# Kernel tuning notes

Measured on AMD Instinct MI355X. Metric: run time of the kernel, lower is better.

Reference implementation:

```python
import jax, jax.numpy as jnp
import numpy as np

B, S, D_IN, D_H, D_OUT, NB = 4, 4096, 1024, 1024, 1024, 8
BD = D_H // NB  # block size of the block-diagonal gate projections
R_MIN, R_MAX, EPS = 0.9, 0.999, 1e-8


def setup_inputs() -> dict:
    key = jax.random.key(0)
    ks = jax.random.split(key, 8)
    x = jax.random.normal(ks[0], (B, S, D_IN), dtype=jnp.float32)
    h0 = jnp.zeros((B, D_H), dtype=jnp.float32)
    # input projection Dense(d_hidden)
    W_in = jax.random.normal(ks[1], (D_IN, D_H), dtype=jnp.float32) / np.sqrt(D_IN)
    b_in = jnp.zeros((D_H,), dtype=jnp.float32)
    # two BlockDiagonalLinear gate projections (n_blocks blocks of [BD, BD])
    Wgx = jax.random.normal(ks[2], (NB, BD, BD), dtype=jnp.float32) / np.sqrt(BD)
    bgx = jnp.zeros((D_H,), dtype=jnp.float32)
    Wga = jax.random.normal(ks[3], (NB, BD, BD), dtype=jnp.float32) / np.sqrt(BD)
    bga = jnp.zeros((D_H,), dtype=jnp.float32)
    # stable_init_real: softplus(param) == -log(r) with r ~ U[r_min, r_max] in magnitude
    u = jax.random.uniform(ks[4], (D_H,), dtype=jnp.float32)
    a_real = 0.5 * jnp.log(u * (R_MAX**2 - R_MIN**2) + R_MIN**2 + EPS)
    a_real_param = jnp.log(jnp.exp(-a_real) - 1.0)
    # output projection Dense(d_out)
    W_out = jax.random.normal(ks[5], (D_H, D_OUT), dtype=jnp.float32) / np.sqrt(D_H)
    b_out = jnp.zeros((D_OUT,), dtype=jnp.float32)
    return dict(x=x, h0=h0, W_in=W_in, b_in=b_in, Wgx=Wgx, bgx=bgx,
                Wga=Wga, bga=bga, a_real_param=a_real_param,
                W_out=W_out, b_out=b_out)


def _block_diag_linear(x, W, b):
    # x: [B,S,D_H] -> split into NB blocks of BD, per-block matmul
    xb = x.reshape(x.shape[0], x.shape[1], NB, BD)
    y = jnp.einsum('bsni,nio->bsno', xb, W)
    return y.reshape(x.shape[0], x.shape[1], D_H) + b


def reference(x, h0, W_in, b_in, Wgx, bgx, Wga, bga, a_real_param, W_out, b_out):
    # input projection
    x = x @ W_in + b_in  # [B,S,D_H]
    # input-dependent gates (sigmoid of block-diagonal projections)
    gate_x = jax.nn.sigmoid(_block_diag_linear(x, Wgx, bgx))
    gate_a = jax.nn.sigmoid(_block_diag_linear(x, Wga, bga))
    # real-only RG-LRU recurrence coefficient: a = exp(-8 * gate_a * softplus(c))
    log_a = -8.0 * gate_a * jax.nn.softplus(a_real_param)  # [B,S,D_H], <= 0
    a = jnp.exp(log_a)
    # gated input with sqrt(1 - a^2) normalization (sqrt_bound_derivative fwd == sqrt)
    gx = gate_x * x * jnp.sqrt(1.0 - jnp.exp(2.0 * log_a))
    # fold initial state into the first step: h_1 = a_1 * h0 + gx_1
    gx = gx.at[:, 0].add(a[:, 0] * h0)
    # linear scan h_t = a_t * h_{t-1} + gx_t via associative scan over seq axis
    def combine(c1, c2):
        a1, x1 = c1
        a2, x2 = c2
        return (a2 * a1, a2 * x1 + x2)
    _, h = jax.lax.associative_scan(combine, (a, gx), axis=1)  # [B,S,D_H]
    out = h @ W_out + b_out  # [B,S,D_OUT]
    return out, h[:, -1]
```

## Files before the change

### kernel.cpp

```cpp
#include <hip/hip_runtime.h>

#define B_SZ 4
#define SEQ 4096
#define DIN 1024
#define DH 1024
#define DOUT 1024
#define NBLK 8
#define MTOK (B_SZ * SEQ)
#define CHUNK 64
#define NCHUNK (SEQ / CHUNK)

typedef _Float16 half8 __attribute__((ext_vector_type(8)));
typedef _Float16 half4v __attribute__((ext_vector_type(4)));
typedef float f32x4 __attribute__((ext_vector_type(4)));

union HPack { unsigned int u; _Float16 h[2]; };

__device__ __forceinline__ void gl_lds16(const void* g, void* l) {
  __builtin_amdgcn_global_load_lds((__attribute__((address_space(1))) void*)g,
                                   (__attribute__((address_space(3))) void*)l,
                                   16, 0, 0);
}

__device__ __forceinline__ int swz_h(int r, int c) {
  return (((r << 8) | (c << 1)) ^ ((r & 7) << 4)) >> 1;
}

__global__ __launch_bounds__(256)
void prep_kernel(const float* __restrict__ Win, const float* __restrict__ Wout,
                 const float* __restrict__ Wgx, const float* __restrict__ Wga,
                 _Float16* __restrict__ WinT, _Float16* __restrict__ WoutT,
                 _Float16* __restrict__ WgxT, _Float16* __restrict__ WgaT) {
  __shared__ float tile[64][65];
  int t = blockIdx.x;
  const float* src; _Float16* dst; int C; size_t bo = 0;
  if (t < 256)      { src = Win;  dst = WinT;  C = 1024; }
  else if (t < 512) { src = Wout; dst = WoutT; C = 1024; t -= 256; }
  else if (t < 544) { int u = t - 512; src = Wgx; dst = WgxT; C = 128;
                      bo = (size_t)(u >> 2) * (128 * 128); t = u & 3; }
  else              { int u = t - 544; src = Wga; dst = WgaT; C = 128;
                      bo = (size_t)(u >> 2) * (128 * 128); t = u & 3; }
  const int nbx = C >> 6;
  const int r0 = (t / nbx) * 64, c0 = (t % nbx) * 64;
  const int tr = threadIdx.x >> 6, tc = threadIdx.x & 63;
#pragma unroll
  for (int i = 0; i < 64; i += 4)
    tile[tr + i][tc] = src[bo + (size_t)(r0 + tr + i) * C + c0 + tc];
  __syncthreads();
#pragma unroll
  for (int i = 0; i < 64; i += 4) {
    const int cc = i + tr;
    dst[bo + (size_t)(c0 + cc) * C + r0 + tc] = (_Float16)tile[tc][cc];
  }
}

template <int OUT_F32>
__global__ __launch_bounds__(256, 4)
void gemm_bt(const _Float16* __restrict__ A, const _Float16* __restrict__ Bt,
             const float* __restrict__ bias, void* __restrict__ C,
             int M, int N, int K) {
  __shared__ __align__(16) _Float16 As[128 * 64];
  __shared__ __align__(16) _Float16 Bs[128 * 64];
  const int tid = threadIdx.x;
  const int wave = tid >> 6, lane = tid & 63;
  const int m0 = blockIdx.x * 128, n0 = blockIdx.y * 128;
  const int wm = (wave >> 1) * 64, wn = (wave & 1) * 64;
  const int row = lane & 15, quad = lane >> 4;
  const int srow = lane >> 3, scol = (lane & 7) * 8;

  f32x4 acc[4][4] = {};
#pragma unroll 1
  for (int kt = 0; kt < K; kt += 64) {
#pragma unroll
    for (int ci = 0; ci < 4; ci++) {
      const int c = wave * 4 + ci;
      gl_lds16(A  + (size_t)(m0 + c * 8 + srow) * K + kt + scol, As + c * 512);
      gl_lds16(Bt + (size_t)(n0 + c * 8 + srow) * K + kt + scol, Bs + c * 512);
    }
    __syncthreads();
#pragma unroll
    for (int kk = 0; kk < 64; kk += 32) {
      half8 af[4], bf[4];
#pragma unroll
      for (int i = 0; i < 4; i++)
        af[i] = *(const half8*)&As[(wm + i * 16 + row) * 64 + kk + quad * 8];
#pragma unroll
      for (int i = 0; i < 4; i++)
        bf[i] = *(const half8*)&Bs[(wn + i * 16 + row) * 64 + kk + quad * 8];
#pragma unroll
      for (int i = 0; i < 4; i++)
#pragma unroll
        for (int j = 0; j < 4; j++)
          acc[i][j] = __builtin_amdgcn_mfma_f32_16x16x32_f16(af[i], bf[j], acc[i][j], 0, 0, 0);
    }
    __syncthreads();
  }
  float bv[4];
#pragma unroll
  for (int j = 0; j < 4; j++) bv[j] = bias[n0 + wn + j * 16 + row];
#pragma unroll
  for (int i = 0; i < 4; i++) {
#pragma unroll
    for (int r = 0; r < 4; r++) {
      const int m = m0 + wm + i * 16 + quad * 4 + r;
      const size_t base = (size_t)m * N + n0 + wn + row;
#pragma unroll
      for (int j = 0; j < 4; j++) {
        const float v = acc[i][j][r] + bv[j];
        if (OUT_F32) ((float*)C)[base + j * 16] = v;
        else         ((_Float16*)C)[base + j * 16] = (_Float16)v;
      }
    }
  }
}

__global__ __launch_bounds__(256, 4)
void gemm1_gates(const float* __restrict__ Ax, const _Float16* __restrict__ Bt,
                 const float* __restrict__ bias,
                 const _Float16* __restrict__ WxT, const _Float16* __restrict__ WaT,
                 const float* __restrict__ bgx, const float* __restrict__ bga,
                 const float* __restrict__ arp,
                 unsigned int* __restrict__ ag,
                 float* __restrict__ cA, float* __restrict__ cH) {
  __shared__ __align__(16) _Float16 smem[128 * 128];
  _Float16* const As = smem;
  _Float16* const Bs = smem + 128 * 64;
  const int tid = threadIdx.x;
  const int wave = tid >> 6, lane = tid & 63;
  const int m0 = blockIdx.x * 128, nb = blockIdx.y, n0 = nb * 128;
  const int wm = (wave >> 1) * 64, wn = (wave & 1) * 64;
  const int row = lane & 15, quad = lane >> 4;
  const int srow = lane >> 3, scol = (lane & 7) * 8;

  f32x4 acc[4][4] = {};
#pragma unroll 1
  for (int kt = 0; kt < DIN; kt += 64) {
#pragma unroll
    for (int ci = 0; ci < 4; ci++) {
      const int c = wave * 4 + ci;
      gl_lds16(Bt + (size_t)(n0 + c * 8 + srow) * DIN + kt + scol, Bs + c * 512);
    }
#pragma unroll
    for (int ci = 0; ci < 4; ci++) {
      const int c = wave * 4 + ci;
      const float* s = Ax + (size_t)(m0 + c * 8 + srow) * DIN + kt + scol;
      const float4 t0 = ((const float4*)s)[0];
      const float4 t1 = ((const float4*)s)[1];
      half8 hv;
      hv[0] = (_Float16)t0.x; hv[1] = (_Float16)t0.y;
      hv[2] = (_Float16)t0.z; hv[3] = (_Float16)t0.w;
      hv[4] = (_Float16)t1.x; hv[5] = (_Float16)t1.y;
      hv[6] = (_Float16)t1.z; hv[7] = (_Float16)t1.w;
      *(half8*)&As[c * 512 + lane * 8] = hv;
    }
    __syncthreads();
#pragma unroll
    for (int kk = 0; kk < 64; kk += 32) {
      half8 af[4], bf[4];
#pragma unroll
      for (int i = 0; i < 4; i++)
        af[i] = *(const half8*)&As[(wm + i * 16 + row) * 64 + kk + quad * 8];
#pragma unroll
      for (int i = 0; i < 4; i++)
        bf[i] = *(const half8*)&Bs[(wn + i * 16 + row) * 64 + kk + quad * 8];
#pragma unroll
      for (int i = 0; i < 4; i++)
#pragma unroll
        for (int j = 0; j < 4; j++)
          acc[i][j] = __builtin_amdgcn_mfma_f32_16x16x32_f16(af[i], bf[j], acc[i][j], 0, 0, 0);
    }
    __syncthreads();
  }

  {
    float bv[4];
#pragma unroll
    for (int j = 0; j < 4; j++) bv[j] = bias[n0 + wn + j * 16 + row];
#pragma unroll
    for (int i = 0; i < 4; i++)
#pragma unroll
      for (int r = 0; r < 4; r++) {
        const int tl = wm + i * 16 + quad * 4 + r;
#pragma unroll
        for (int j = 0; j < 4; j++)
          smem[swz_h(tl, wn + j * 16 + row)] = (_Float16)(acc[i][j][r] + bv[j]);
      }
  }
  __syncthreads();

  const _Float16* const WxB = WxT + (size_t)nb * (128 * 128);
  const _Float16* const WaB = WaT + (size_t)nb * (128 * 128);
  const int b_idx = (m0 + wm) >> 12;
  const int c_idx = ((m0 + wm) & (SEQ - 1)) >> 6;
  const int cbase = c_idx * (B_SZ * DH) + b_idx * DH + n0 + wn + row;
  const size_t agbase = ((size_t)(blockIdx.x * NBLK + nb) * 4 + wave) * 4096;

#pragma unroll 1
  for (int jp = 0; jp < 2; jp++) {
    f32x4 accx[4][2] = {}, acca[4][2] = {};
#pragma unroll
    for (int kk = 0; kk < 128; kk += 32) {
      half8 af[4];
#pragma unroll
      for (int i = 0; i < 4; i++)
        af[i] = *(const half8*)&smem[swz_h(wm + i * 16 + row, kk + quad * 8)];
#pragma unroll
      for (int jj = 0; jj < 2; jj++) {
        const size_t wo = (size_t)(wn + (jp * 2 + jj) * 16 + row) * 128 + kk + quad * 8;
        const half8 bx = *(const half8*)&WxB[wo];
        const half8 ba = *(const half8*)&WaB[wo];
#pragma unroll
        for (int i = 0; i < 4; i++) {
          accx[i][jj] = __builtin_amdgcn_mfma_f32_16x16x32_f16(af[i], bx, accx[i][jj], 0, 0, 0);
          acca[i][jj] = __builtin_amdgcn_mfma_f32_16x16x32_f16(af[i], ba, acca[i][jj], 0, 0, 0);
        }
      }
    }
    float bxv[2], bav[2], cd[2];
#pragma unroll
    for (int jj = 0; jj < 2; jj++) {
      const int d = n0 + wn + (jp * 2 + jj) * 16 + row;
      bxv[jj] = bgx[d]; bav[jj] = bga[d];
      cd[jj] = log1pf(expf(arp[d]));
    }
    float Arun[2] = {1.f, 1.f}, Hrun[2] = {0.f, 0.f};
#pragma unroll
    for (int i = 0; i < 4; i++) {
      float Aseg[2] = {1.f, 1.f}, Hseg[2] = {0.f, 0.f};
#pragma unroll
      for (int r = 0; r < 4; r++) {
        const int tl = wm + i * 16 + quad * 4 + r;
#pragma unroll
        for (int jj = 0; jj < 2; jj++) {
          const float px = accx[i][jj][r] + bxv[jj];
          const float pa = acca[i][jj][r] + bav[jj];
          const float sx = 1.f / (1.f + __expf(-px));
          const float sa = 1.f / (1.f + __expf(-pa));
          const float a = __expf(-8.f * sa * cd[jj]);
          const float n2 = fmaxf(1.f - a * a, 0.f);
          const float xv = (float)smem[swz_h(tl, wn + (jp * 2 + jj) * 16 + row)];
          HPack pk;
          pk.h[0] = (_Float16)a;
          pk.h[1] = (_Float16)(sx * xv * sqrtf(n2));
          ag[agbase + (size_t)(((i * 4 + r) * 4) + jp * 2 + jj) * 64 + lane] = pk.u;
          const float ar = (float)pk.h[0], gr = (float)pk.h[1];
          Aseg[jj] *= ar;
          Hseg[jj] = fmaf(ar, Hseg[jj], gr);
        }
      }
#pragma unroll
      for (int jj = 0; jj < 2; jj++) {
        float A1 = Aseg[jj], H1 = Hseg[jj];
        float A2 = __shfl_down(A1, 16, 64), H2 = __shfl_down(H1, 16, 64);
        H1 = fmaf(A2, H1, H2); A1 *= A2;
        A2 = __shfl_down(A1, 32, 64); H2 = __shfl_down(H1, 32, 64);
        H1 = fmaf(A2, H1, H2); A1 *= A2;
        Hrun[jj] = fmaf(A1, Hrun[jj], H1);
        Arun[jj] *= A1;
      }
    }
    if (lane < 16) {
#pragma unroll
      for (int jj = 0; jj < 2; jj++) {
        cA[cbase + (jp * 2 + jj) * 16] = Arun[jj];
        cH[cbase + (jp * 2 + jj) * 16] = Hrun[jj];
      }
    }
  }
}

__global__ __launch_bounds__(256)
void scan_p2(const float* __restrict__ cA, const float* __restrict__ cH,
             const float* __restrict__ h0, float* __restrict__ cin,
             float* __restrict__ hlast) {
  const int wave = threadIdx.x >> 6, lane = threadIdx.x & 63;
  const int g = blockIdx.x * 4 + wave;
  float A = cA[(size_t)lane * (B_SZ * DH) + g], H = cH[(size_t)lane * (B_SZ * DH) + g];
#pragma unroll
  for (int d = 1; d < 64; d <<= 1) {
    const float Ap = __shfl_up(A, d, 64), Hp = __shfl_up(H, d, 64);
    if (lane >= d) { H = fmaf(A, Hp, H); A *= Ap; }
  }
  const float h0g = h0[g];
  if (lane == 63) hlast[g] = fmaf(A, h0g, H);
  float Ae = __shfl_up(A, 1, 64), He = __shfl_up(H, 1, 64);
  if (lane == 0) { Ae = 1.f; He = 0.f; }
  cin[(size_t)lane * (B_SZ * DH) + g] = fmaf(Ae, h0g, He);
}

__global__ __launch_bounds__(256)
void scan_p3(const unsigned int* __restrict__ ag,
             const float* __restrict__ cin, _Float16* __restrict__ h) {
  const int gtid = blockIdx.x * 256 + threadIdx.x;
  const int d = gtid & (DH - 1);
  const int bc = gtid >> 10;
  const int b = bc >> 6, c = bc & (NCHUNK - 1);
  const int mblk = b * 32 + (c >> 1), wmb = c & 1;
  const int nb = d >> 7, wnb = (d >> 6) & 1, j = (d >> 4) & 3, row = d & 15;
  const size_t agb = ((size_t)(mblk * NBLK + nb) * 4 + wmb * 2 + wnb) * 4096
                   + j * 64 + row;
  const size_t hbase = ((size_t)(b * SEQ + c * CHUNK)) * DH + d;
  float carry = cin[c * (B_SZ * DH) + b * DH + d];
#pragma unroll 8
  for (int t = 0; t < CHUNK; t++) {
    HPack pk;
    pk.u = ag[agb + (size_t)(((t >> 4) * 4 + (t & 3)) * 4) * 64 + ((t >> 2) & 3) * 16];
    const float av = (float)pk.h[0];
    const float gv = (float)pk.h[1];
    carry = fmaf(av, carry, gv);
    h[hbase + (size_t)t * DH] = (_Float16)carry;
  }
}

extern "C" void kernel_launch(void* const* d_in, const int* in_sizes, int n_in,
                              void* d_out, int out_size, void* d_ws, size_t ws_size,
                              hipStream_t stream) {
  const float* x     = (const float*)d_in[0];
  const float* h0    = (const float*)d_in[1];
  const float* W_in  = (const float*)d_in[2];
  const float* b_in  = (const float*)d_in[3];
  const float* Wgx   = (const float*)d_in[4];
  const float* bgx   = (const float*)d_in[5];
  const float* Wga   = (const float*)d_in[6];
  const float* bga   = (const float*)d_in[7];
  const float* arp   = (const float*)d_in[8];
  const float* W_out = (const float*)d_in[9];
  const float* b_out = (const float*)d_in[10];
  float* out = (float*)d_out;
  float* hlast = out + (size_t)MTOK * DOUT;

  char* p = (char*)d_ws;
  auto take = [&](size_t bytes) { char* r = p; p += (bytes + 255) & ~(size_t)255; return r; };
  _Float16* h_buf = (_Float16*)take((size_t)MTOK * DH * 2);
  unsigned int* ag = (unsigned int*)take((size_t)MTOK * DH * 4);
  _Float16* WinT  = (_Float16*)take((size_t)DIN * DH * 2);
  _Float16* WoutT = (_Float16*)take((size_t)DH * DOUT * 2);
  _Float16* WgxT  = (_Float16*)take((size_t)NBLK * 128 * 128 * 2);
  _Float16* WgaT  = (_Float16*)take((size_t)NBLK * 128 * 128 * 2);
  float* cA   = (float*)take((size_t)NCHUNK * B_SZ * DH * 4);
  float* cH   = (float*)take((size_t)NCHUNK * B_SZ * DH * 4);
  float* cin  = (float*)take((size_t)NCHUNK * B_SZ * DH * 4);

  prep_kernel<<<576, 256, 0, stream>>>(W_in, W_out, Wgx, Wga,
                                       WinT, WoutT, WgxT, WgaT);
  gemm1_gates<<<dim3(MTOK / 128, NBLK), 256, 0, stream>>>(
      x, WinT, b_in, WgxT, WgaT, bgx, bga, arp, ag, cA, cH);
  scan_p2<<<(B_SZ * DH) / 4, 256, 0, stream>>>(cA, cH, h0, cin, hlast);
  scan_p3<<<(B_SZ * NCHUNK * DH) / 256, 256, 0, stream>>>(ag, cin, h_buf);
  gemm_bt<1><<<dim3(MTOK / 128, DOUT / 128), 256, 0, stream>>>(h_buf, WoutT, b_out, out, MTOK, DOUT, DH);
}
```

Baseline: 306.7 us.

## Double-buffer GEMM K-loop with prefetch and XOR-swizzled LDS layout

Both GEMM kernels now use two LDS buffers with a 32-wide K step, issuing the next tile's global loads before computing on the current tile. The LDS rows are 32 halves with an XOR slot swizzle to reduce bank conflicts on fragment reads. In the gates kernel the fp32 activation loads are issued early and converted/stored after the MFMAs to hide latency. This trades a smaller K tile per iteration, and more loop overhead, for overlap of memory and compute.

```diff
diff --git a/kernel.cpp b/kernel.cpp
--- a/kernel.cpp
+++ b/kernel.cpp
@@ -59,41 +59,51 @@
 void gemm_bt(const _Float16* __restrict__ A, const _Float16* __restrict__ Bt,
              const float* __restrict__ bias, void* __restrict__ C,
              int M, int N, int K) {
-  __shared__ __align__(16) _Float16 As[128 * 64];
-  __shared__ __align__(16) _Float16 Bs[128 * 64];
+  __shared__ __align__(16) _Float16 smem[16384];
   const int tid = threadIdx.x;
   const int wave = tid >> 6, lane = tid & 63;
   const int m0 = blockIdx.x * 128, n0 = blockIdx.y * 128;
   const int wm = (wave >> 1) * 64, wn = (wave & 1) * 64;
   const int row = lane & 15, quad = lane >> 4;
-  const int srow = lane >> 3, scol = (lane & 7) * 8;
+  const int srow = lane >> 2;
+  const int ssl  = ((lane & 3) ^ (srow & 3)) * 8;
+  const int sslot = (quad ^ (row & 3)) * 8;
 
   f32x4 acc[4][4] = {};
+#pragma unroll
+  for (int ci = 0; ci < 2; ci++) {
+    const int c = wave * 2 + ci;
+    gl_lds16(A  + (size_t)(m0 + c * 16 + srow) * K + ssl, smem + c * 512);
+    gl_lds16(Bt + (size_t)(n0 + c * 16 + srow) * K + ssl, smem + 8192 + c * 512);
+  }
+  __syncthreads();
+
+  int co = 0;
 #pragma unroll 1
-  for (int kt = 0; kt < K; kt += 64) {
-#pragma unroll
-    for (int ci = 0; ci < 4; ci++) {
-      const int c = wave * 4 + ci;
-      gl_lds16(A  + (size_t)(m0 + c * 8 + srow) * K + kt + scol, As + c * 512);
-      gl_lds16(Bt + (size_t)(n0 + c * 8 + srow) * K + kt + scol, Bs + c * 512);
-    }
+  for (int kt = 0; kt < K; kt += 32) {
+    const int nx = co ^ 4096;
+    if (kt + 32 < K) {
+#pragma unroll
+      for (int ci = 0; ci < 2; ci++) {
+        const int c = wave * 2 + ci;
+        gl_lds16(A  + (size_t)(m0 + c * 16 + srow) * K + kt + 32 + ssl, smem + nx + c * 512);
+        gl_lds16(Bt + (size_t)(n0 + c * 16 + srow) * K + kt + 32 + ssl, smem + 8192 + nx + c * 512);
+      }
+    }
+    half8 af[4], bf[4];
+#pragma unroll
+    for (int i = 0; i < 4; i++)
+      af[i] = *(const half8*)&smem[co + (wm + i * 16 + row) * 32 + sslot];
+#pragma unroll
+    for (int j = 0; j < 4; j++)
+      bf[j] = *(const half8*)&smem[8192 + co + (wn + j * 16 + row) * 32 + sslot];
+#pragma unroll
+    for (int i = 0; i < 4; i++)
+#pragma unroll
+      for (int j = 0; j < 4; j++)
+        acc[i][j] = __builtin_amdgcn_mfma_f32_16x16x32_f16(af[i], bf[j], acc[i][j], 0, 0, 0);
     __syncthreads();
-#pragma unroll
-    for (int kk = 0; kk < 64; kk += 32) {
-      half8 af[4], bf[4];
-#pragma unroll
-      for (int i = 0; i < 4; i++)
-        af[i] = *(const half8*)&As[(wm + i * 16 + row) * 64 + kk + quad * 8];
-#pragma unroll
-      for (int i = 0; i < 4; i++)
-        bf[i] = *(const half8*)&Bs[(wn + i * 16 + row) * 64 + kk + quad * 8];
-#pragma unroll
-      for (int i = 0; i < 4; i++)
-#pragma unroll
-        for (int j = 0; j < 4; j++)
-          acc[i][j] = __builtin_amdgcn_mfma_f32_16x16x32_f16(af[i], bf[j], acc[i][j], 0, 0, 0);
-    }
-    __syncthreads();
+    co = nx;
   }
   float bv[4];
 #pragma unroll
@@ -122,54 +132,74 @@
                  const float* __restrict__ arp,
                  unsigned int* __restrict__ ag,
                  float* __restrict__ cA, float* __restrict__ cH) {
-  __shared__ __align__(16) _Float16 smem[128 * 128];
-  _Float16* const As = smem;
-  _Float16* const Bs = smem + 128 * 64;
+  __shared__ __align__(16) _Float16 smem[16384];
   const int tid = threadIdx.x;
   const int wave = tid >> 6, lane = tid & 63;
   const int m0 = blockIdx.x * 128, nb = blockIdx.y, n0 = nb * 128;
   const int wm = (wave >> 1) * 64, wn = (wave & 1) * 64;
   const int row = lane & 15, quad = lane >> 4;
-  const int srow = lane >> 3, scol = (lane & 7) * 8;
+  const int srow = lane >> 2;
+  const int ssl  = ((lane & 3) ^ (srow & 3)) * 8;
+  const int sslot = (quad ^ (row & 3)) * 8;
+  const int c0 = wave * 2, c1 = c0 + 1;
+  const size_t arow0 = (size_t)(m0 + c0 * 16 + srow) * DIN + ssl;
+  const size_t arow1 = (size_t)(m0 + c1 * 16 + srow) * DIN + ssl;
 
   f32x4 acc[4][4] = {};
+  gl_lds16(Bt + (size_t)(n0 + c0 * 16 + srow) * DIN + ssl, smem + 8192 + c0 * 512);
+  gl_lds16(Bt + (size_t)(n0 + c1 * 16 + srow) * DIN + ssl, smem + 8192 + c1 * 512);
+  {
+    const float4 t0 = *(const float4*)(Ax + arow0);
+    const float4 t1 = *(const float4*)(Ax + arow0 + 4);
+    const float4 t2 = *(const float4*)(Ax + arow1);
+    const float4 t3 = *(const float4*)(Ax + arow1 + 4);
+    half8 h0, h1;
+    h0[0] = (_Float16)t0.x; h0[1] = (_Float16)t0.y; h0[2] = (_Float16)t0.z; h0[3] = (_Float16)t0.w;
+    h0[4] = (_Float16)t1.x; h0[5] = (_Float16)t1.y; h0[6] = (_Float16)t1.z; h0[7] = (_Float16)t1.w;
+    h1[0] = (_Float16)t2.x; h1[1] = (_Float16)t2.y; h1[2] = (_Float16)t2.z; h1[3] = (_Float16)t2.w;
+    h1[4] = (_Float16)t3.x; h1[5] = (_Float16)t3.y; h1[6] = (_Float16)t3.z; h1[7] = (_Float16)t3.w;
+    *(half8*)&smem[c0 * 512 + lane * 8] = h0;
+    *(half8*)&smem[c1 * 512 + lane * 8] = h1;
+  }
+  __syncthreads();
+
+  int co = 0;
 #pragma unroll 1
-  for (int kt = 0; kt < DIN; kt += 64) {
-#pragma unroll
-    for (int ci = 0; ci < 4; ci++) {
-      const int c = wave * 4 + ci;
-      gl_lds16(Bt + (size_t)(n0 + c * 8 + srow) * DIN + kt + scol, Bs + c * 512);
-    }
-#pragma unroll
-    for (int ci = 0; ci < 4; ci++) {
-      const int c = wave * 4 + ci;
-      const float* s = Ax + (size_t)(m0 + c * 8 + srow) * DIN + kt + scol;
-      const float4 t0 = ((const float4*)s)[0];
-      const float4 t1 = ((const float4*)s)[1];
-      half8 hv;
-      hv[0] = (_Float16)t0.x; hv[1] = (_Float16)t0.y;
-      hv[2] = (_Float16)t0.z; hv[3] = (_Float16)t0.w;
-      hv[4] = (_Float16)t1.x; hv[5] = (_Float16)t1.y;
-      hv[6] = (_Float16)t1.z; hv[7] = (_Float16)t1.w;
-      *(half8*)&As[c * 512 + lane * 8] = hv;
+  for (int kt = 0; kt < DIN; kt += 32) {
+    const int nx = co ^ 4096;
+    const bool pf = (kt + 32 < DIN);
+    float4 t0 = {}, t1 = {}, t2 = {}, t3 = {};
+    if (pf) {
+      gl_lds16(Bt + (size_t)(n0 + c0 * 16 + srow) * DIN + kt + 32 + ssl, smem + 8192 + nx + c0 * 512);
+      gl_lds16(Bt + (size_t)(n0 + c1 * 16 + srow) * DIN + kt + 32 + ssl, smem + 8192 + nx + c1 * 512);
+      t0 = *(const float4*)(Ax + arow0 + kt + 32);
+      t1 = *(const float4*)(Ax + arow0 + kt + 36);
+      t2 = *(const float4*)(Ax + arow1 + kt + 32);
+      t3 = *(const float4*)(Ax + arow1 + kt + 36);
+    }
+    half8 af[4], bf[4];
+#pragma unroll
+    for (int i = 0; i < 4; i++)
+      af[i] = *(const half8*)&smem[co + (wm + i * 16 + row) * 32 + sslot];
+#pragma unroll
+    for (int j = 0; j < 4; j++)
+      bf[j] = *(const half8*)&smem[8192 + co + (wn + j * 16 + row) * 32 + sslot];
+#pragma unroll
+    for (int i = 0; i < 4; i++)
+#pragma unroll
+      for (int j = 0; j < 4; j++)
+        acc[i][j] = __builtin_amdgcn_mfma_f32_16x16x32_f16(af[i], bf[j], acc[i][j], 0, 0, 0);
+    if (pf) {
+      half8 h0, h1;
+      h0[0] = (_Float16)t0.x; h0[1] = (_Float16)t0.y; h0[2] = (_Float16)t0.z; h0[3] = (_Float16)t0.w;
+      h0[4] = (_Float16)t1.x; h0[5] = (_Float16)t1.y; h0[6] = (_Float16)t1.z; h0[7] = (_Float16)t1.w;
+      h1[0] = (_Float16)t2.x; h1[1] = (_Float16)t2.y; h1[2] = (_Float16)t2.z; h1[3] = (_Float16)t2.w;
+      h1[4] = (_Float16)t3.x; h1[5] = (_Float16)t3.y; h1[6] = (_Float16)t3.z; h1[7] = (_Float16)t3.w;
+      *(half8*)&smem[nx + c0 * 512 + lane * 8] = h0;
+      *(half8*)&smem[nx + c1 * 512 + lane * 8] = h1;
     }
     __syncthreads();
-#pragma unroll
-    for (int kk = 0; kk < 64; kk += 32) {
-      half8 af[4], bf[4];
-#pragma unroll
-      for (int i = 0; i < 4; i++)
-        af[i] = *(const half8*)&As[(wm + i * 16 + row) * 64 + kk + quad * 8];
-#pragma unroll
-      for (int i = 0; i < 4; i++)
-        bf[i] = *(const half8*)&Bs[(wn + i * 16 + row) * 64 + kk + quad * 8];
-#pragma unroll
-      for (int i = 0; i < 4; i++)
-#pragma unroll
-        for (int j = 0; j < 4; j++)
-          acc[i][j] = __builtin_amdgcn_mfma_f32_16x16x32_f16(af[i], bf[j], acc[i][j], 0, 0, 0);
-    }
-    __syncthreads();
+    co = nx;
   }
 
   {
```

After: 302.2 us. Within noise of the previous version (-1.5%).
